# Optimization experiments

Measured on AMD Instinct MI355X. Metric: run time of the kernel, lower is better.

The kernel has to match this reference:

```python
import jax, jax.numpy as jnp
import numpy as np

D_MODEL = 1024
NUM_HEADS = 16
D_HEAD = D_MODEL // NUM_HEADS
MAX_LEN = 16384
BATCH = 4
SEQ = 1024


def setup_inputs() -> dict:
    key = jax.random.key(0)
    ks = jax.random.split(key, 10)
    s = 1.0 / np.sqrt(D_MODEL)
    return {
        "q_in": jax.random.normal(ks[0], (BATCH, SEQ, D_MODEL), jnp.float32),
        "k_in": jax.random.normal(ks[1], (BATCH, SEQ, D_MODEL), jnp.float32),
        "v_in": jax.random.normal(ks[2], (BATCH, SEQ, D_MODEL), jnp.float32),
        "Wq": jax.random.normal(ks[3], (D_MODEL, D_MODEL), jnp.float32) * s,
        "bq": jnp.zeros((D_MODEL,), jnp.float32),
        "Wk": jax.random.normal(ks[4], (D_MODEL, D_MODEL), jnp.float32) * s,
        "bk": jnp.zeros((D_MODEL,), jnp.float32),
        "Wv": jax.random.normal(ks[5], (D_MODEL, D_MODEL), jnp.float32) * s,
        "bv": jnp.zeros((D_MODEL,), jnp.float32),
        "Er": jax.random.normal(ks[6], (MAX_LEN, D_HEAD), jnp.float32),
    }


def _skew(QEr):
    # QEr: [B, H, S, S] -> pad one zero column on the left, reshape, drop row 0
    B, H, S, _ = QEr.shape
    padded = jnp.pad(QEr, ((0, 0), (0, 0), (0, 0), (1, 0)))  # [B,H,S,S+1]
    reshaped = padded.reshape(B, H, S + 1, S)
    return reshaped[:, :, 1:, :]  # [B,H,S,S]


def reference(q_in, k_in, v_in, Wq, bq, Wk, bk, Wv, bv, Er):
    B, S, _ = q_in.shape
    H, Dh = NUM_HEADS, D_HEAD
    # projections, split into heads: [B, H, S, Dh]
    q = (q_in @ Wq + bq).reshape(B, S, H, Dh).transpose(0, 2, 1, 3)
    k = (k_in @ Wk + bk).reshape(B, S, H, Dh).transpose(0, 2, 1, 3)
    v = (v_in @ Wv + bv).reshape(B, S, H, Dh).transpose(0, 2, 1, 3)
    # relative position scores: Er slice [S, Dh]
    Er_sl = Er[MAX_LEN - S:, :]
    QEr = jnp.einsum('bhsd,td->bhst', q, Er_sl)  # [B,H,S,S]
    Srel = _skew(QEr)
    QK = jnp.einsum('bhsd,bhtd->bhst', q, k)
    attn = (QK + Srel) / jnp.sqrt(jnp.asarray(Dh, q.dtype))
    attn = jax.nn.softmax(attn, axis=-1)
    out = jnp.einsum('bhst,bhtd->bhsd', attn, v)  # [B,H,S,Dh]
    out = out.transpose(0, 2, 1, 3).reshape(B, S, H * Dh)
    return out
```

## Files before the change

kernel.cpp:

```cpp
#include <hip/hip_runtime.h>
#include <hip/hip_bf16.h>
#include <cstdint>

#define S_LEN 1024
#define DMODEL 1024
#define NHEADS 16
#define DHEAD 64
#define MAXLEN 16384
#define BATCH 4

typedef __attribute__((ext_vector_type(8))) short bf16x8;
typedef __attribute__((ext_vector_type(4))) float f32x4;

#define AS1(p) ((const __attribute__((address_space(1))) unsigned int*)(p))
#define AS3(p) ((__attribute__((address_space(3))) unsigned int*)(p))

__device__ inline unsigned short f2b(float f) {
  unsigned int u = __float_as_uint(f);
  unsigned int r = (u + 0x7FFFu + ((u >> 16) & 1u)) >> 16;
  return (unsigned short)r;
}
__device__ inline float b2f(unsigned short u) {
  return __uint_as_float(((unsigned int)u) << 16);
}

#define LDSWZ(row, slot) (((row) << 6) + (((slot) ^ ((row) & 7)) << 3))

__global__ __launch_bounds__(256) void wt_convert3(
    const float* __restrict__ W0, const float* __restrict__ W1, const float* __restrict__ W2,
    unsigned short* __restrict__ T0, unsigned short* __restrict__ T1, unsigned short* __restrict__ T2) {
  const float* W = (blockIdx.z == 0) ? W0 : (blockIdx.z == 1) ? W1 : W2;
  unsigned short* WT = (blockIdx.z == 0) ? T0 : (blockIdx.z == 1) ? T1 : T2;
  __shared__ float t[32][33];
  const int bi = blockIdx.y * 32, bj = blockIdx.x * 32;
  const int r = threadIdx.x >> 3, c4 = (threadIdx.x & 7) * 4;
  float4 f = *(const float4*)&W[(size_t)(bi + r) * DMODEL + bj + c4];
  t[r][c4] = f.x; t[r][c4 + 1] = f.y; t[r][c4 + 2] = f.z; t[r][c4 + 3] = f.w;
  __syncthreads();
  ushort4 u;
  u.x = f2b(t[c4][r]); u.y = f2b(t[c4 + 1][r]);
  u.z = f2b(t[c4 + 2][r]); u.w = f2b(t[c4 + 3][r]);
  *(ushort4*)&WT[(size_t)(bj + r) * DMODEL + bi + c4] = u;
}

__global__ __launch_bounds__(256) void xconvert3(
    const float* __restrict__ X0, const float* __restrict__ X1, const float* __restrict__ X2,
    unsigned short* __restrict__ B0, unsigned short* __restrict__ B1, unsigned short* __restrict__ B2) {
  const int z = blockIdx.z;
  const float* X = (z == 0) ? X0 : (z == 1) ? X1 : X2;
  unsigned short* B = (z == 0) ? B0 : (z == 1) ? B1 : B2;
  size_t i = ((size_t)blockIdx.x * 256 + threadIdx.x) * 16;
  union { unsigned short h[16]; int4 v[2]; } u;
#pragma unroll
  for (int r = 0; r < 4; ++r) {
    float4 f = *(const float4*)(X + i + r * 4);
    u.h[r * 4 + 0] = f2b(f.x); u.h[r * 4 + 1] = f2b(f.y);
    u.h[r * 4 + 2] = f2b(f.z); u.h[r * 4 + 3] = f2b(f.w);
  }
  *(int4*)(B + i) = u.v[0];
  *(int4*)(B + i + 8) = u.v[1];
}

__global__ __launch_bounds__(256) void er_convert(const float* __restrict__ Er,
                                                  unsigned short* __restrict__ Erb) {
  const int i = blockIdx.x * 1024 + threadIdx.x * 4;
  float4 f = *(const float4*)(Er + (size_t)(MAXLEN - S_LEN) * DHEAD + i);
  Erb[i] = f2b(f.x); Erb[i + 1] = f2b(f.y); Erb[i + 2] = f2b(f.z); Erb[i + 3] = f2b(f.w);
}

__global__ __launch_bounds__(256) void proj_glds3(
    const unsigned short* __restrict__ Xq, const unsigned short* __restrict__ Xk,
    const unsigned short* __restrict__ Xv,
    const unsigned short* __restrict__ T0, const unsigned short* __restrict__ T1,
    const unsigned short* __restrict__ T2,
    const float* __restrict__ b0, const float* __restrict__ b1, const float* __restrict__ b2,
    unsigned short* __restrict__ O0, unsigned short* __restrict__ O1,
    unsigned short* __restrict__ O2) {
  const int z = blockIdx.z;
  const unsigned short* X = (z == 0) ? Xq : (z == 1) ? Xk : Xv;
  const unsigned short* WT = (z == 0) ? T0 : (z == 1) ? T1 : T2;
  const float* bias = (z == 0) ? b0 : (z == 1) ? b1 : b2;
  unsigned short* Out = (z == 0) ? O0 : (z == 1) ? O1 : O2;
  __shared__ unsigned short As[128 * 64];
  __shared__ unsigned short Bs[128 * 64];
  const int tid = threadIdx.x;
  const int l = tid & 63, w = tid >> 6;
  const int o = blockIdx.y * 8 + blockIdx.x;
  const int lid = (o & 7) * 32 + (o >> 3);
  const int bm = (lid >> 3) * 128, bn = (lid & 7) * 128;
  const int wr = (w >> 1) * 64, wc = (w & 1) * 64;
  const int lrow = l >> 3;
  const int slotlog = (l & 7) ^ (lrow & 7);
  const unsigned short* Xa = X + (size_t)(bm + lrow) * DMODEL + slotlog * 8;
  const unsigned short* Wa = WT + (size_t)(bn + lrow) * DMODEL + slotlog * 8;
  f32x4 acc[4][4] = {};
  for (int k0 = 0; k0 < DMODEL; k0 += 64) {
    __syncthreads();
#pragma unroll
    for (int j = 0; j < 4; ++j) {
      int r8 = (w * 4 + j) * 8;
      __builtin_amdgcn_global_load_lds(AS1(Xa + (size_t)r8 * DMODEL + k0),
                                       AS3(&As[(w * 4 + j) * 512]), 16, 0, 0);
      __builtin_amdgcn_global_load_lds(AS1(Wa + (size_t)r8 * DMODEL + k0),
                                       AS3(&Bs[(w * 4 + j) * 512]), 16, 0, 0);
    }
    __syncthreads();
#pragma unroll
    for (int ks = 0; ks < 2; ++ks) {
      bf16x8 a[4], b[4];
#pragma unroll
      for (int f = 0; f < 4; ++f) {
        int row = wr + f * 16 + (l & 15);
        a[f] = *(const bf16x8*)&As[LDSWZ(row, ks * 4 + (l >> 4))];
        int col = wc + f * 16 + (l & 15);
        b[f] = *(const bf16x8*)&Bs[LDSWZ(col, ks * 4 + (l >> 4))];
      }
#pragma unroll
      for (int i = 0; i < 4; ++i)
#pragma unroll
        for (int j = 0; j < 4; ++j)
          acc[i][j] = __builtin_amdgcn_mfma_f32_16x16x32_bf16(a[i], b[j], acc[i][j], 0, 0, 0);
    }
  }
#pragma unroll
  for (int i = 0; i < 4; ++i) {
    int m = bm + wr + i * 16 + ((l >> 4) << 2);
#pragma unroll
    for (int j = 0; j < 4; ++j) {
      int n = bn + wc + j * 16 + (l & 15);
      float bv = bias[n];
#pragma unroll
      for (int e = 0; e < 4; ++e)
        Out[(size_t)(m + e) * DMODEL + n] = f2b(acc[i][j][e] + bv);
    }
  }
}

__global__ __launch_bounds__(256) void g_diag_zero(unsigned short* __restrict__ G) {
  int s = blockIdx.x * 256 + threadIdx.x;
  if (s < S_LEN - 1)
    G[(size_t)blockIdx.y * S_LEN * S_LEN + (size_t)s * S_LEN + s + 1] = 0;
}

__global__ __launch_bounds__(256) void qer_mfma(const unsigned short* __restrict__ qp,
    const unsigned short* __restrict__ Erb, unsigned short* __restrict__ G, int bh0) {
  const int bh = bh0 + blockIdx.z;
  const int b = bh >> 4, h = bh & 15;
  __shared__ unsigned short As[128 * 64];
  __shared__ unsigned short Bs[128 * 64];
  const int tid = threadIdx.x, l = tid & 63, wid = tid >> 6;
  const int bm = blockIdx.y * 128, bn = blockIdx.x * 128;
  const int wr = (wid >> 1) * 64, wc = (wid & 1) * 64;
  const unsigned short* qb = qp + (size_t)b * S_LEN * DMODEL + h * DHEAD;
  unsigned short* Gc = G + (size_t)blockIdx.z * S_LEN * S_LEN;
#pragma unroll
  for (int r = 0; r < 4; ++r) {
    int s = r * 256 + tid;
    int row = s >> 3, sl = s & 7;
    *(int4*)&As[LDSWZ(row, sl)] = *(const int4*)(qb + (size_t)(bm + row) * DMODEL + sl * 8);
    *(int4*)&Bs[LDSWZ(row, sl)] = *(const int4*)(Erb + (size_t)(bn + row) * DHEAD + sl * 8);
  }
  __syncthreads();
  f32x4 acc[4][4] = {};
#pragma unroll
  for (int ks = 0; ks < 2; ++ks) {
    bf16x8 a[4], b[4];
#pragma unroll
    for (int f = 0; f < 4; ++f) {
      int row = wr + f * 16 + (l & 15);
      a[f] = *(const bf16x8*)&As[LDSWZ(row, ks * 4 + (l >> 4))];
      int col = wc + f * 16 + (l & 15);
      b[f] = *(const bf16x8*)&Bs[LDSWZ(col, ks * 4 + (l >> 4))];
    }
#pragma unroll
    for (int i = 0; i < 4; ++i)
#pragma unroll
      for (int j = 0; j < 4; ++j)
        acc[i][j] = __builtin_amdgcn_mfma_f32_16x16x32_bf16(a[i], b[j], acc[i][j], 0, 0, 0);
  }
#pragma unroll
  for (int i = 0; i < 4; ++i) {
    int m = bm + wr + i * 16 + ((l >> 4) << 2);
#pragma unroll
    for (int j = 0; j < 4; ++j) {
      int n = bn + wc + j * 16 + (l & 15);
#pragma unroll
      for (int e = 0; e < 4; ++e) {
        int s = m + e;
        int hi = (n >= 1023 - s);
        int r_ = hi ? s : s - 1;
        int t_ = hi ? (n + s - 1023) : (n + s + 1);
        if (r_ >= 0)
          Gc[(size_t)r_ * S_LEN + t_] = f2b(acc[i][j][e]);
      }
    }
  }
}

__global__ __launch_bounds__(256) void attn_skew(const unsigned short* __restrict__ qp,
    const unsigned short* __restrict__ kp, const unsigned short* __restrict__ vp,
    const unsigned short* __restrict__ G, float* __restrict__ out, int bh0) {
  const int bh = bh0 + blockIdx.y;
  const int b = bh >> 4, h = bh & 15;
  const int s0 = blockIdx.x * 64;
  __shared__ unsigned short Qs[64 * 64];
  __shared__ unsigned short Ks[64 * 64];
  __shared__ unsigned short Vt[64 * 64];
  __shared__ unsigned short Ps[4][16 * 64];
  const int tid = threadIdx.x, l = tid & 63, w = tid >> 6;
  const int lg = l >> 4, li = l & 15;
  const unsigned short* qb = qp + (size_t)b * S_LEN * DMODEL + h * DHEAD;
  const unsigned short* kb = kp + (size_t)b * S_LEN * DMODEL + h * DHEAD;
  const unsigned short* vb = vp + (size_t)b * S_LEN * DMODEL + h * DHEAD;
  const unsigned short* Gb = G + (size_t)blockIdx.y * S_LEN * S_LEN;

#pragma unroll
  for (int r = 0; r < 2; ++r) {
    int s = r * 256 + tid;
    int row = s >> 3, sl = s & 7;
    *(int4*)&Qs[LDSWZ(row, sl)] = *(const int4*)(qb + (size_t)(s0 + row) * DMODEL + sl * 8);
  }
  __syncthreads();
  bf16x8 qf[2];
#pragma unroll
  for (int ks = 0; ks < 2; ++ks)
    qf[ks] = *(const bf16x8*)&Qs[LDSWZ(w * 16 + li, ks * 4 + lg)];

  f32x4 o4[4] = {};
  float m_r[4] = {-1e30f, -1e30f, -1e30f, -1e30f};
  float l_r[4] = {0.f, 0.f, 0.f, 0.f};
  int sg[4];
  const unsigned short* gp[4];
#pragma unroll
  for (int i = 0; i < 4; ++i) {
    sg[i] = s0 + w * 16 + (lg << 2) + i;
    gp[i] = Gb + (size_t)sg[i] * S_LEN + li;
  }
  const int pr = tid & 31, dh0 = (tid >> 5) * 8;

  for (int ti = 0; ti < 16; ++ti) {
    const int t0 = ti * 64;
    __syncthreads();
#pragma unroll
    for (int r = 0; r < 2; ++r) {
      int s = r * 256 + tid; int row = s >> 3, sl = s & 7;
      *(int4*)&Ks[LDSWZ(row, sl)] = *(const int4*)(kb + (size_t)(t0 + row) * DMODEL + sl * 8);
    }
    {
      const unsigned short* v0p = vb + (size_t)(t0 + pr * 2) * DMODEL + dh0;
      union { int4 v; unsigned short hh[8]; } va, vc;
      va.v = *(const int4*)v0p;
      vc.v = *(const int4*)(v0p + DMODEL);
      unsigned int* vtw = (unsigned int*)Vt;
#pragma unroll
      for (int j = 0; j < 8; ++j) {
        int dh = dh0 + j;
        int widx = dh * 32 + (((pr >> 2) ^ (dh & 7)) << 2) + (pr & 3);
        vtw[widx] = (unsigned int)va.hh[j] | ((unsigned int)vc.hh[j] << 16);
      }
    }
    __syncthreads();
    unsigned short rv[4][4];
#pragma unroll
    for (int f = 0; f < 4; ++f)
#pragma unroll
      for (int i = 0; i < 4; ++i)
        rv[f][i] = gp[i][t0 + f * 16];
    f32x4 sa[4] = {};
#pragma unroll
    for (int ks = 0; ks < 2; ++ks)
#pragma unroll
      for (int f = 0; f < 4; ++f) {
        bf16x8 kf = *(const bf16x8*)&Ks[LDSWZ(f * 16 + li, ks * 4 + lg)];
        sa[f] = __builtin_amdgcn_mfma_f32_16x16x32_bf16(qf[ks], kf, sa[f], 0, 0, 0);
      }
    float tmax[4] = {-1e30f, -1e30f, -1e30f, -1e30f};
#pragma unroll
    for (int f = 0; f < 4; ++f) {
#pragma unroll
      for (int i = 0; i < 4; ++i) {
        float sv = (sa[f][i] + b2f(rv[f][i])) * 0.125f;
        sa[f][i] = sv;
        tmax[i] = fmaxf(tmax[i], sv);
      }
    }
#pragma unroll
    for (int off = 8; off >= 1; off >>= 1)
#pragma unroll
      for (int i = 0; i < 4; ++i) tmax[i] = fmaxf(tmax[i], __shfl_xor(tmax[i], off));
    float scale[4];
#pragma unroll
    for (int i = 0; i < 4; ++i) {
      float mn = fmaxf(m_r[i], tmax[i]);
      scale[i] = __expf(m_r[i] - mn);
      m_r[i] = mn;
    }
    float psum[4] = {0.f, 0.f, 0.f, 0.f};
    unsigned short* Pw = &Ps[w][0];
#pragma unroll
    for (int f = 0; f < 4; ++f) {
#pragma unroll
      for (int i = 0; i < 4; ++i) {
        float pv = __expf(sa[f][i] - m_r[i]);
        psum[i] += pv;
        int prow = (lg << 2) + i, pcol = f * 16 + li;
        Pw[LDSWZ(prow, pcol >> 3) + (pcol & 7)] = f2b(pv);
      }
    }
#pragma unroll
    for (int off = 8; off >= 1; off >>= 1)
#pragma unroll
      for (int i = 0; i < 4; ++i) psum[i] += __shfl_xor(psum[i], off);
#pragma unroll
    for (int i = 0; i < 4; ++i) l_r[i] = l_r[i] * scale[i] + psum[i];
#pragma unroll
    for (int f = 0; f < 4; ++f)
#pragma unroll
      for (int i = 0; i < 4; ++i) o4[f][i] *= scale[i];
#pragma unroll
    for (int ks = 0; ks < 2; ++ks) {
      bf16x8 pf = *(const bf16x8*)&Pw[LDSWZ(li, ks * 4 + lg)];
#pragma unroll
      for (int f = 0; f < 4; ++f) {
        bf16x8 vf = *(const bf16x8*)&Vt[LDSWZ(f * 16 + li, ks * 4 + lg)];
        o4[f] = __builtin_amdgcn_mfma_f32_16x16x32_bf16(pf, vf, o4[f], 0, 0, 0);
      }
    }
  }
#pragma unroll
  for (int i = 0; i < 4; ++i) {
    float inv = 1.f / l_r[i];
#pragma unroll
    for (int f = 0; f < 4; ++f)
      out[(size_t)(b * S_LEN + sg[i]) * DMODEL + h * DHEAD + f * 16 + li] = o4[f][i] * inv;
  }
}

extern "C" void kernel_launch(void* const* d_in, const int* in_sizes, int n_in,
                              void* d_out, int out_size, void* d_ws, size_t ws_size,
                              hipStream_t stream) {
  (void)in_sizes; (void)n_in; (void)out_size;
  const float* q_in = (const float*)d_in[0];
  const float* k_in = (const float*)d_in[1];
  const float* v_in = (const float*)d_in[2];
  const float* Wq   = (const float*)d_in[3];
  const float* bq   = (const float*)d_in[4];
  const float* Wk   = (const float*)d_in[5];
  const float* bk   = (const float*)d_in[6];
  const float* Wv   = (const float*)d_in[7];
  const float* bv   = (const float*)d_in[8];
  const float* Er   = (const float*)d_in[9];
  float* out = (float*)d_out;

  char* ws = (char*)d_ws;
  const size_t MB = (size_t)1 << 20;
  unsigned short* wtq = (unsigned short*)(ws);
  unsigned short* wtk = (unsigned short*)(ws + 2 * MB);
  unsigned short* wtv = (unsigned short*)(ws + 4 * MB);
  unsigned short* erb = (unsigned short*)(ws + 6 * MB);
  unsigned short* qp  = (unsigned short*)(ws + 8 * MB);
  unsigned short* kp  = (unsigned short*)(ws + 16 * MB);
  unsigned short* vp  = (unsigned short*)(ws + 24 * MB);
  unsigned short* xq  = (unsigned short*)(ws + 32 * MB);
  unsigned short* xk  = (unsigned short*)(ws + 40 * MB);
  unsigned short* xv  = (unsigned short*)(ws + 48 * MB);
  unsigned short* G   = (unsigned short*)(ws + 56 * MB);

  const size_t gavail = (ws_size > 56 * MB) ? (ws_size - 56 * MB) : 0;
  int chunk = (int)(gavail / (2 * MB));
  if (chunk < 1) chunk = 1;
  if (chunk > 64) chunk = 64;

  dim3 blk(256);
  hipLaunchKernelGGL(wt_convert3, dim3(32, 32, 3), blk, 0, stream,
                     Wq, Wk, Wv, wtq, wtk, wtv);
  hipLaunchKernelGGL(xconvert3, dim3(1024, 1, 3), blk, 0, stream,
                     q_in, k_in, v_in, xq, xk, xv);
  hipLaunchKernelGGL(er_convert, dim3(64), blk, 0, stream, Er, erb);

  dim3 gproj(DMODEL / 128, (BATCH * S_LEN) / 128, 3);
  hipLaunchKernelGGL(proj_glds3, gproj, blk, 0, stream,
                     xq, xk, xv, wtq, wtk, wtv, bq, bk, bv, qp, kp, vp);

  for (int bh0 = 0; bh0 < BATCH * NHEADS; bh0 += chunk) {
    int nb = BATCH * NHEADS - bh0;
    if (nb > chunk) nb = chunk;
    hipLaunchKernelGGL(g_diag_zero, dim3(4, nb), blk, 0, stream, G);
    dim3 gqer(S_LEN / 128, S_LEN / 128, nb);
    hipLaunchKernelGGL(qer_mfma, gqer, blk, 0, stream, qp, erb, G, bh0);
    dim3 gattn(S_LEN / 64, nb);
    hipLaunchKernelGGL(attn_skew, gattn, blk, 0, stream, qp, kp, vp, G, out, bh0);
  }
}
```

Measured before the change: 180.5 us.

## Stage K and skew tile through LDS via direct global-to-LDS loads

K tiles and the precomputed relative-position (skewed) score tile G are now loaded with global_load_lds directly into a unified LDS buffer instead of going through registers. Previously each lane did scattered 2-byte global reads of G, which were poorly coalesced. G is now fetched as coalesced 16-byte rows and read back from swizzled LDS. The Q staging region is reused for the P buffers to keep the LDS footprint the same. The change relies on the XOR swizzle matching LDSWZ and on the async LDS writes being complete at the existing barrier.

After: 190.8 us. +5.7%, slower.

```diff
diff --git a/kernel.cpp b/kernel.cpp
--- a/kernel.cpp
+++ b/kernel.cpp
@@ -203,10 +203,8 @@
   const int bh = bh0 + blockIdx.y;
   const int b = bh >> 4, h = bh & 15;
   const int s0 = blockIdx.x * 64;
-  __shared__ unsigned short Qs[64 * 64];
-  __shared__ unsigned short Ks[64 * 64];
-  __shared__ unsigned short Vt[64 * 64];
-  __shared__ unsigned short Ps[4][16 * 64];
+  __shared__ unsigned short lds[16384];
+  const int KS = 0, VT = 4096, GS = 8192, QP = 12288;
   const int tid = threadIdx.x, l = tid & 63, w = tid >> 6;
   const int lg = l >> 4, li = l & 15;
   const unsigned short* qb = qp + (size_t)b * S_LEN * DMODEL + h * DHEAD;
@@ -218,40 +216,48 @@
   for (int r = 0; r < 2; ++r) {
     int s = r * 256 + tid;
     int row = s >> 3, sl = s & 7;
-    *(int4*)&Qs[LDSWZ(row, sl)] = *(const int4*)(qb + (size_t)(s0 + row) * DMODEL + sl * 8);
+    *(int4*)&lds[QP + LDSWZ(row, sl)] =
+        *(const int4*)(qb + (size_t)(s0 + row) * DMODEL + sl * 8);
   }
   __syncthreads();
   bf16x8 qf[2];
 #pragma unroll
   for (int ks = 0; ks < 2; ++ks)
-    qf[ks] = *(const bf16x8*)&Qs[LDSWZ(w * 16 + li, ks * 4 + lg)];
+    qf[ks] = *(const bf16x8*)&lds[QP + LDSWZ(w * 16 + li, ks * 4 + lg)];
+
+  const int lrow = l >> 3;
+  const int chk = (l & 7) ^ lrow;
+  const unsigned short* Ka = kb + (size_t)(w * 8 + lrow) * DMODEL + chk * 8;
+  const unsigned short* Ga = Gb + (size_t)(s0 + w * 8 + lrow) * S_LEN + chk * 8;
+  const int pr = tid & 31, dh0 = (tid >> 5) * 8;
 
   f32x4 o4[4] = {};
   float m_r[4] = {-1e30f, -1e30f, -1e30f, -1e30f};
   float l_r[4] = {0.f, 0.f, 0.f, 0.f};
-  int sg[4];
-  const unsigned short* gp[4];
+  int sg[4], rloc[4], gbase[4];
 #pragma unroll
   for (int i = 0; i < 4; ++i) {
     sg[i] = s0 + w * 16 + (lg << 2) + i;
-    gp[i] = Gb + (size_t)sg[i] * S_LEN + li;
-  }
-  const int pr = tid & 31, dh0 = (tid >> 5) * 8;
+    rloc[i] = w * 16 + (lg << 2) + i;
+    gbase[i] = GS + rloc[i] * 64;
+  }
 
   for (int ti = 0; ti < 16; ++ti) {
     const int t0 = ti * 64;
     __syncthreads();
 #pragma unroll
-    for (int r = 0; r < 2; ++r) {
-      int s = r * 256 + tid; int row = s >> 3, sl = s & 7;
-      *(int4*)&Ks[LDSWZ(row, sl)] = *(const int4*)(kb + (size_t)(t0 + row) * DMODEL + sl * 8);
+    for (int j = 0; j < 2; ++j) {
+      __builtin_amdgcn_global_load_lds(AS1(Ka + (size_t)(t0 + j * 32) * DMODEL),
+                                       AS3(&lds[KS + (j * 256 + w * 64) * 8]), 16, 0, 0);
+      __builtin_amdgcn_global_load_lds(AS1(Ga + (size_t)j * 32 * S_LEN + t0),
+                                       AS3(&lds[GS + (j * 256 + w * 64) * 8]), 16, 0, 0);
     }
     {
       const unsigned short* v0p = vb + (size_t)(t0 + pr * 2) * DMODEL + dh0;
       union { int4 v; unsigned short hh[8]; } va, vc;
       va.v = *(const int4*)v0p;
       vc.v = *(const int4*)(v0p + DMODEL);
-      unsigned int* vtw = (unsigned int*)Vt;
+      unsigned int* vtw = (unsigned int*)(lds + VT);
 #pragma unroll
       for (int j = 0; j < 8; ++j) {
         int dh = dh0 + j;
@@ -260,26 +266,22 @@
       }
     }
     __syncthreads();
-    unsigned short rv[4][4];
-#pragma unroll
-    for (int f = 0; f < 4; ++f)
-#pragma unroll
-      for (int i = 0; i < 4; ++i)
-        rv[f][i] = gp[i][t0 + f * 16];
     f32x4 sa[4] = {};
 #pragma unroll
     for (int ks = 0; ks < 2; ++ks)
 #pragma unroll
       for (int f = 0; f < 4; ++f) {
-        bf16x8 kf = *(const bf16x8*)&Ks[LDSWZ(f * 16 + li, ks * 4 + lg)];
+        bf16x8 kf = *(const bf16x8*)&lds[KS + LDSWZ(f * 16 + li, ks * 4 + lg)];
         sa[f] = __builtin_amdgcn_mfma_f32_16x16x32_bf16(qf[ks], kf, sa[f], 0, 0, 0);
       }
     float tmax[4] = {-1e30f, -1e30f, -1e30f, -1e30f};
 #pragma unroll
     for (int f = 0; f < 4; ++f) {
+      int cc = f * 2 + (li >> 3), c7 = li & 7;
 #pragma unroll
       for (int i = 0; i < 4; ++i) {
-        float sv = (sa[f][i] + b2f(rv[f][i])) * 0.125f;
+        unsigned short rvv = lds[gbase[i] + ((cc ^ (rloc[i] & 7)) << 3) + c7];
+        float sv = (sa[f][i] + b2f(rvv)) * 0.125f;
         sa[f][i] = sv;
         tmax[i] = fmaxf(tmax[i], sv);
       }
@@ -296,7 +298,7 @@
       m_r[i] = mn;
     }
     float psum[4] = {0.f, 0.f, 0.f, 0.f};
-    unsigned short* Pw = &Ps[w][0];
+    unsigned short* Pw = lds + QP + w * 1024;
 #pragma unroll
     for (int f = 0; f < 4; ++f) {
 #pragma unroll
@@ -322,7 +324,7 @@
       bf16x8 pf = *(const bf16x8*)&Pw[LDSWZ(li, ks * 4 + lg)];
 #pragma unroll
       for (int f = 0; f < 4; ++f) {
-        bf16x8 vf = *(const bf16x8*)&Vt[LDSWZ(f * 16 + li, ks * 4 + lg)];
+        bf16x8 vf = *(const bf16x8*)&lds[VT + LDSWZ(f * 16 + li, ks * 4 + lg)];
         o4[f] = __builtin_amdgcn_mfma_f32_16x16x32_bf16(pf, vf, o4[f], 0, 0, 0);
       }
     }
```
